# Performance work log

Hardware: AMD Instinct MI355X
Metric: run time of the kernel (lower is better)

## Reference

```python
import jax, jax.numpy as jnp
import numpy as np
import math

D, H, DK, DFF, B, T, K = 512, 8, 64, 2048, 8, 512, 31
P = 2 * T - 1  # rel-pos length


def _ln(x, g, b, eps=1e-5):
    mu = jnp.mean(x, -1, keepdims=True)
    var = jnp.var(x, -1, keepdims=True)
    return (x - mu) * jax.lax.rsqrt(var + eps) * g + b


def _silu(x):
    return x * jax.nn.sigmoid(x)


def _rel_shift(x):
    # x: [B,H,T,P] -> NeMo-style relative shift
    b, h, t, p = x.shape
    x = jnp.pad(x, ((0, 0), (0, 0), (0, 0), (1, 0)))
    x = x.reshape(b, h, p + 1, t)
    return x[:, :, 1:, :].reshape(b, h, t, p)


def _forward(x, pos_emb, ln1_g, ln1_b, ff1_w1, ff1_b1, ff1_w2, ff1_b2,
             lna_g, lna_b, wq, bq, wk, bk, wv, bv, wo, bo, wpos, pbu, pbv,
             lnc_g, lnc_b, pw1_w, pw1_b, dw_w, dw_b, cln_g, cln_b, pw2_w, pw2_b,
             ln2_g, ln2_b, ff2_w1, ff2_b1, ff2_w2, ff2_b2, lno_g, lno_b):
    b, t, d = x.shape
    h, dk = pbu.shape
    # FF1 (half-step residual)
    r = x
    y = _ln(x, ln1_g, ln1_b)
    y = _silu(y @ ff1_w1 + ff1_b1) @ ff1_w2 + ff1_b2
    r = r + 0.5 * y
    # Rel-pos multi-head attention
    y = _ln(r, lna_g, lna_b)
    q = (y @ wq + bq).reshape(b, t, h, dk)
    k = (y @ wk + bk).reshape(b, t, h, dk)
    v = (y @ wv + bv).reshape(b, t, h, dk)
    p = (pos_emb @ wpos).reshape(pos_emb.shape[0], -1, h, dk)[0]  # [P,H,dk]
    ac = jnp.einsum('bthd,bshd->bhts', q + pbu, k)
    bd = jnp.einsum('bthd,phd->bhtp', q + pbv, p)
    bd = _rel_shift(bd)[..., :t]
    attn = jax.nn.softmax((ac + bd) / math.sqrt(dk), axis=-1)
    o = jnp.einsum('bhts,bshd->bthd', attn, v).reshape(b, t, d) @ wo + bo
    r = r + o
    # Conformer convolution module (layer_norm variant)
    y = _ln(r, lnc_g, lnc_b)
    y = y @ pw1_w + pw1_b                       # [B,T,2D] pointwise conv1
    a, g = jnp.split(y, 2, axis=-1)
    y = a * jax.nn.sigmoid(g)                   # GLU over channels
    y = jnp.transpose(y, (0, 2, 1))             # [B,D,T]
    pad = (dw_w.shape[1] - 1) // 2
    y = jax.lax.conv_general_dilated(
        y, dw_w[:, None, :], (1,), [(pad, pad)],
        feature_group_count=d, dimension_numbers=('NCH', 'OIH', 'NCH'))
    y = y + dw_b[None, :, None]
    y = jnp.transpose(y, (0, 2, 1))             # [B,T,D]
    y = _ln(y, cln_g, cln_b)
    y = _silu(y) @ pw2_w + pw2_b                # pointwise conv2
    r = r + y
    # FF2 (half-step residual)
    y = _ln(r, ln2_g, ln2_b)
    y = _silu(y @ ff2_w1 + ff2_b1) @ ff2_w2 + ff2_b2
    r = r + 0.5 * y
    return _ln(r, lno_g, lno_b)


def setup_inputs() -> dict:
    key = jax.random.key(0)
    ks = iter(jax.random.split(key, 64))
    rn = lambda shape, s=0.05: jax.random.normal(next(ks), shape, dtype=jnp.float32) * s
    ones = lambda n: jnp.ones((n,), jnp.float32)
    zeros = lambda n: jnp.zeros((n,), jnp.float32)
    return dict(
        x=jax.random.normal(next(ks), (B, T, D), jnp.float32),
        pos_emb=jax.random.normal(next(ks), (1, P, D), jnp.float32),
        ln1_g=ones(D), ln1_b=zeros(D),
        ff1_w1=rn((D, DFF)), ff1_b1=zeros(DFF), ff1_w2=rn((DFF, D)), ff1_b2=zeros(D),
        lna_g=ones(D), lna_b=zeros(D),
        wq=rn((D, D)), bq=zeros(D), wk=rn((D, D)), bk=zeros(D),
        wv=rn((D, D)), bv=zeros(D), wo=rn((D, D)), bo=zeros(D),
        wpos=rn((D, D)), pbu=rn((H, DK)), pbv=rn((H, DK)),
        lnc_g=ones(D), lnc_b=zeros(D),
        pw1_w=rn((D, 2 * D)), pw1_b=zeros(2 * D),
        dw_w=rn((D, K)), dw_b=zeros(D),
        cln_g=ones(D), cln_b=zeros(D),
        pw2_w=rn((D, D)), pw2_b=zeros(D),
        ln2_g=ones(D), ln2_b=zeros(D),
        ff2_w1=rn((D, DFF)), ff2_b1=zeros(DFF), ff2_w2=rn((DFF, D)), ff2_b2=zeros(D),
        lno_g=ones(D), lno_b=zeros(D))


def reference(x, pos_emb, ln1_g, ln1_b, ff1_w1, ff1_b1, ff1_w2, ff1_b2,
              lna_g, lna_b, wq, bq, wk, bk, wv, bv, wo, bo, wpos, pbu, pbv,
              lnc_g, lnc_b, pw1_w, pw1_b, dw_w, dw_b, cln_g, cln_b, pw2_w, pw2_b,
              ln2_g, ln2_b, ff2_w1, ff2_b1, ff2_w2, ff2_b2, lno_g, lno_b):
    return _forward(x, pos_emb, ln1_g, ln1_b, ff1_w1, ff1_b1, ff1_w2, ff1_b2,
                    lna_g, lna_b, wq, bq, wk, bk, wv, bv, wo, bo, wpos, pbu, pbv,
                    lnc_g, lnc_b, pw1_w, pw1_b, dw_w, dw_b, cln_g, cln_b, pw2_w, pw2_b,
                    ln2_g, ln2_b, ff2_w1, ff2_b1, ff2_w2, ff2_b2, lno_g, lno_b)
```

## Files before the change

### kernel.cpp

```cpp
#include <hip/hip_runtime.h>
#include <hip/hip_bf16.h>

#define Bb 8
#define Tt 512
#define Dd 512
#define Hh 8
#define DKk 64
#define DFFf 2048
#define Pp 1023
#define KCc 31
#define BTt 4096
#define QS 1536

typedef __hip_bfloat16 bf16;
typedef __attribute__((ext_vector_type(8))) short short8;
typedef __attribute__((ext_vector_type(4))) short s4v;
typedef __attribute__((ext_vector_type(4))) float f32x4;

union BFU { __hip_bfloat16 h; short s; };
static __device__ __forceinline__ short bfbits(float f) {
    BFU u; u.h = __float2bfloat16(f); return u.s;
}
static __device__ __forceinline__ float bff(short s) {
    BFU u; u.s = s; return __bfloat162float(u.h);
}
static __device__ __forceinline__ unsigned pk2(float a, float b) {
    return (unsigned)(unsigned short)bfbits(a) | ((unsigned)(unsigned short)bfbits(b) << 16);
}

static __device__ __forceinline__ int dflag(const void* lg) {
    return ((const unsigned*)lg)[0] == 0x3F803F80u;
}

#define GLD16(g, l) __builtin_amdgcn_global_load_lds(                          \
    (const __attribute__((address_space(1))) void*)(g),                        \
    (__attribute__((address_space(3))) void*)(l), 16, 0, 0)

#define XCD_SWZ(bxs, bys)                                                     \
    int nwg_ = gridDim.x * gridDim.y;                                         \
    int w_ = blockIdx.y * gridDim.x + blockIdx.x;                             \
    int sw_ = (w_ & 7) * (nwg_ >> 3) + (w_ >> 3);                             \
    int bxs = sw_ % gridDim.x, bys = sw_ / gridDim.x;

struct CvtDesc { const void* src; unsigned n; unsigned off; unsigned startBlk; };
struct CvtArgs { CvtDesc d[32]; };

__global__ __launch_bounds__(256) void cvt_batch_k(CvtArgs args, int ncv,
                                                   bf16* __restrict__ dst,
                                                   const void* __restrict__ lg) {
    int bid = blockIdx.x;
    int ti = 0;
    while (ti + 1 < ncv && bid >= (int)args.d[ti + 1].startBlk) ti++;
    CvtDesc de = args.d[ti];
    unsigned i = (bid - de.startBlk) * 256u + threadIdx.x;
    if (i >= de.n) return;
    float v;
    if (dflag(lg)) v = __bfloat162float(((const bf16*)de.src)[i]);
    else           v = ((const float*)de.src)[i];
    dst[de.off + i] = __float2bfloat16(v);
}

struct TD { const void* src; unsigned doff, R, C, startBlk; };
struct TArgs { TD d[11]; };

__global__ __launch_bounds__(256) void transpose_batch_k(TArgs ta, bf16* __restrict__ wt,
                                                         const void* __restrict__ lg) {
    int bid = blockIdx.x;
    int ti = 0;
    while (ti + 1 < 11 && bid >= (int)ta.d[ti + 1].startBlk) ti++;
    TD t = ta.d[ti];
    int tile = bid - t.startBlk;
    int ntc = t.C >> 5;
    int tr = tile / ntc, tc = tile % ntc;
    __shared__ short tl[32][33];
    short* out = (short*)wt + t.doff;
    int tx = threadIdx.x & 31, ty = threadIdx.x >> 5;
    int fl = dflag(lg);
#pragma unroll
    for (int i = 0; i < 32; i += 8) {
        size_t idx = (size_t)(tr * 32 + ty + i) * t.C + tc * 32 + tx;
        short v;
        if (fl) v = ((const short*)t.src)[idx];
        else    v = bfbits(((const float*)t.src)[idx]);
        tl[ty + i][tx] = v;
    }
    __syncthreads();
#pragma unroll
    for (int i = 0; i < 32; i += 8)
        out[(size_t)(tc * 32 + ty + i) * t.R + tr * 32 + tx] = tl[tx][ty + i];
}

__global__ __launch_bounds__(256) void prep_misc_k(const void* __restrict__ dww, bf16* __restrict__ dwT,
                                                   const void* __restrict__ bq, const void* __restrict__ bk,
                                                   const void* __restrict__ bv, bf16* __restrict__ bqkv,
                                                   const void* __restrict__ lg) {
    int i = blockIdx.x * 256 + threadIdx.x;
    int fl = dflag(lg);
    if (i < Dd * KCc) {
        int d = i / KCc, j = i % KCc;
        short v = fl ? ((const short*)dww)[i] : bfbits(((const float*)dww)[i]);
        ((short*)dwT)[j * Dd + d] = v;
    } else {
        int j = i - Dd * KCc;
        if (j < QS) {
            const void* s = (j < 512) ? bq : ((j < 1024) ? bk : bv);
            int idx = j & 511;
            short v = fl ? ((const short*)s)[idx] : bfbits(((const float*)s)[idx]);
            ((short*)bqkv)[j] = v;
        }
    }
}

__global__ __launch_bounds__(256) void prep_pf_k(const bf16* __restrict__ pbuf,
                                                 bf16* __restrict__ pF) {
    int h = blockIdx.x >> 6, J = blockIdx.x & 63;
    int idx = threadIdx.x * 4;
    int ksp = idx >> 9;
    int l = (idx >> 3) & 63;
    int e0 = idx & 7;
    int lm = l & 15, qd = l >> 4;
    int prow = J * 16 - 1 + lm;
    s4v v;
    if (prow < 0) {
        v = s4v{0, 0, 0, 0};
    } else {
        v = *(const s4v*)((const short*)pbuf + (size_t)prow * Dd + h * DKk + ksp * 32 + qd * 8 + e0);
    }
    *(s4v*)((short*)pF + ((size_t)h * 64 + J) * 1024 + idx) = v;
}

template <int SILU>
__global__ __launch_bounds__(256) void ln_k(const float* __restrict__ in,
                                            const bf16* __restrict__ g,
                                            const bf16* __restrict__ b,
                                            bf16* __restrict__ out) {
    int row = blockIdx.x;
    int tid = threadIdx.x;
    float2 v = ((const float2*)(in + (size_t)row * Dd))[tid];
    float s = v.x + v.y;
    float ss = v.x * v.x + v.y * v.y;
#pragma unroll
    for (int off = 32; off > 0; off >>= 1) {
        s += __shfl_xor(s, off);
        ss += __shfl_xor(ss, off);
    }
    __shared__ float red[2][4];
    int wid = tid >> 6;
    if ((tid & 63) == 0) { red[0][wid] = s; red[1][wid] = ss; }
    __syncthreads();
    float S = red[0][0] + red[0][1] + red[0][2] + red[0][3];
    float SS = red[1][0] + red[1][1] + red[1][2] + red[1][3];
    float mean = S * (1.0f / Dd);
    float var = SS * (1.0f / Dd) - mean * mean;
    float rstd = rsqrtf(var + 1e-5f);
    unsigned gp = *(const unsigned*)((const short*)g + 2 * tid);
    unsigned bp = *(const unsigned*)((const short*)b + 2 * tid);
    float o0 = (v.x - mean) * rstd * bff((short)(gp & 0xFFFF)) + bff((short)(bp & 0xFFFF));
    float o1 = (v.y - mean) * rstd * bff((short)(gp >> 16)) + bff((short)(bp >> 16));
    if (SILU) {
        o0 = o0 / (1.0f + __expf(-o0));
        o1 = o1 / (1.0f + __expf(-o1));
    }
    *(unsigned*)((short*)out + (size_t)row * Dd + 2 * tid) = pk2(o0, o1);
}

__global__ __launch_bounds__(256) void ln_x_k(const void* __restrict__ x,
                                              const bf16* __restrict__ g,
                                              const bf16* __restrict__ b,
                                              float* __restrict__ r,
                                              bf16* __restrict__ out,
                                              const void* __restrict__ lg) {
    int row = blockIdx.x;
    int tid = threadIdx.x;
    size_t base = (size_t)row * Dd;
    float v0, v1;
    if (dflag(lg)) {
        unsigned xp = *(const unsigned*)((const short*)x + base + 2 * tid);
        v0 = bff((short)(xp & 0xFFFF));
        v1 = bff((short)(xp >> 16));
    } else {
        float2 xv = ((const float2*)((const float*)x + base))[tid];
        v0 = xv.x; v1 = xv.y;
    }
    ((float2*)(r + base))[tid] = make_float2(v0, v1);
    float s = v0 + v1;
    float ss = v0 * v0 + v1 * v1;
#pragma unroll
    for (int off = 32; off > 0; off >>= 1) {
        s += __shfl_xor(s, off);
        ss += __shfl_xor(ss, off);
    }
    __shared__ float red[2][4];
    int wid = tid >> 6;
    if ((tid & 63) == 0) { red[0][wid] = s; red[1][wid] = ss; }
    __syncthreads();
    float S = red[0][0] + red[0][1] + red[0][2] + red[0][3];
    float SS = red[1][0] + red[1][1] + red[1][2] + red[1][3];
    float mean = S * (1.0f / Dd);
    float var = SS * (1.0f / Dd) - mean * mean;
    float rstd = rsqrtf(var + 1e-5f);
    unsigned gp = *(const unsigned*)((const short*)g + 2 * tid);
    unsigned bp = *(const unsigned*)((const short*)b + 2 * tid);
    float o0 = (v0 - mean) * rstd * bff((short)(gp & 0xFFFF)) + bff((short)(bp & 0xFFFF));
    float o1 = (v1 - mean) * rstd * bff((short)(gp >> 16)) + bff((short)(bp >> 16));
    *(unsigned*)((short*)out + base + 2 * tid) = pk2(o0, o1);
}

__global__ __launch_bounds__(256) void ln_out_k(const float* __restrict__ in,
                                                const bf16* __restrict__ g,
                                                const bf16* __restrict__ b,
                                                void* __restrict__ out,
                                                const void* __restrict__ lg) {
    int row = blockIdx.x;
    int tid = threadIdx.x;
    size_t base = (size_t)row * Dd;
    float2 v = ((const float2*)(in + base))[tid];
    float s = v.x + v.y;
    float ss = v.x * v.x + v.y * v.y;
#pragma unroll
    for (int off = 32; off > 0; off >>= 1) {
        s += __shfl_xor(s, off);
        ss += __shfl_xor(ss, off);
    }
    __shared__ float red[2][4];
    int wid = tid >> 6;
    if ((tid & 63) == 0) { red[0][wid] = s; red[1][wid] = ss; }
    __syncthreads();
    float S = red[0][0] + red[0][1] + red[0][2] + red[0][3];
    float SS = red[1][0] + red[1][1] + red[1][2] + red[1][3];
    float mean = S * (1.0f / Dd);
    float var = SS * (1.0f / Dd) - mean * mean;
    float rstd = rsqrtf(var + 1e-5f);
    unsigned gp = *(const unsigned*)((const short*)g + 2 * tid);
    unsigned bp = *(const unsigned*)((const short*)b + 2 * tid);
    float o0 = (v.x - mean) * rstd * bff((short)(gp & 0xFFFF)) + bff((short)(bp & 0xFFFF));
    float o1 = (v.y - mean) * rstd * bff((short)(gp >> 16)) + bff((short)(bp >> 16));
    if (dflag(lg)) {
        *(unsigned*)((short*)out + base + 2 * tid) = pk2(o0, o1);
    } else {
        ((float2*)((float*)out + base))[tid] = make_float2(o0, o1);
    }
}

template <int BM, int BN, int BK, int WM, int WN, typename CT, int ACT, int RES, int VT>
__global__ __launch_bounds__(256) void gemm_mfma_k(const bf16* __restrict__ Abf,
                                                   const bf16* __restrict__ WT,
                                                   const bf16* __restrict__ bias,
                                                   const float* __restrict__ resid,
                                                   CT* __restrict__ C,
                                                   bf16* __restrict__ vt,
                                                   bf16* __restrict__ kf,
                                                   int M, int N, int Kd, float alpha) {
    constexpr int MT = WM / 16, NT = WN / 16;
    constexpr int WX = BN / WN;
    constexpr int CPB = BK / 8;
    constexpr int KS = BK / 32;
    __shared__ __align__(16) short As[BM * BK];
    __shared__ __align__(16) short Bs[BN * BK];
    int tid = threadIdx.x;
    int wid = tid >> 6, lane = tid & 63;
    int lm = lane & 15, quad = lane >> 4;
    int wy = wid / WX, wx = wid % WX;
    XCD_SWZ(bxs, bys);
    int bm = bys * BM, bn = bxs * BN;
    const short* Ag = (const short*)Abf;
    const short* Bg = (const short*)WT;

    f32x4 acc[MT][NT] = {};

    for (int k0 = 0; k0 < Kd; k0 += BK) {
#pragma unroll
        for (int it = 0; it < BM * CPB / 256; it++) {
            int c = it * 256 + tid;
            int row = c / CPB;
            int q = (c % CPB) ^ (row & 7);
            int gr = bm + row;
            if (gr > M - 1) gr = M - 1;
            GLD16(Ag + (size_t)gr * Kd + k0 + q * 8, As + (it * 256 + wid * 64) * 8);
        }
#pragma unroll
        for (int it = 0; it < BN * CPB / 256; it++) {
            int c = it * 256 + tid;
            int row = c / CPB;
            int q = (c % CPB) ^ (row & 7);
            GLD16(Bg + (size_t)(bn + row) * Kd + k0 + q * 8, Bs + (it * 256 + wid * 64) * 8);
        }
        __syncthreads();
        short8 af[MT][KS], bfv[NT][KS];
#pragma unroll
        for (int mt = 0; mt < MT; mt++) {
            int row = wy * WM + mt * 16 + lm;
#pragma unroll
            for (int ks = 0; ks < KS; ks++)
                af[mt][ks] = *(const short8*)&As[row * BK + (((ks * 4 + quad) ^ (row & 7)) * 8)];
        }
#pragma unroll
        for (int nt = 0; nt < NT; nt++) {
            int row = wx * WN + nt * 16 + lm;
#pragma unroll
            for (int ks = 0; ks < KS; ks++)
                bfv[nt][ks] = *(const short8*)&Bs[row * BK + (((ks * 4 + quad) ^ (row & 7)) * 8)];
        }
#pragma unroll
        for (int ks = 0; ks < KS; ks++)
#pragma unroll
            for (int mt = 0; mt < MT; mt++)
#pragma unroll
                for (int nt = 0; nt < NT; nt++)
                    acc[mt][nt] = __builtin_amdgcn_mfma_f32_16x16x32_bf16(af[mt][ks], bfv[nt][ks], acc[mt][nt], 0, 0, 0);
        __syncthreads();
    }

#pragma unroll
    for (int mt = 0; mt < MT; mt++) {
#pragma unroll
        for (int nt = 0; nt < NT; nt++) {
            int gcol = bn + wx * WN + nt * 16 + lm;
            int growb = bm + wy * WM + mt * 16 + quad * 4;
            if (VT && gcol >= 1024) {
                int hd = gcol - 1024;
                int h = hd >> 6, d = hd & 63;
                int b = growb >> 9, tt = growb & 511;
                float bi = bias ? __bfloat162float(bias[gcol]) : 0.f;
                s4v pk;
#pragma unroll
                for (int r = 0; r < 4; r++) pk[r] = bfbits(acc[mt][nt][r] + bi);
                size_t base = (((((size_t)b * 8 + h) * 16 + (tt >> 5)) * 4 + (d >> 4)) * 64 +
                               (((tt >> 3) & 3) * 16 + (d & 15))) * 8 + (tt & 7);
                *(s4v*)((short*)vt + base) = pk;
            } else if (VT && gcol >= 512) {
                int hd = gcol - 512;
                int h = hd >> 6, kk = hd & 63;
                int b = growb >> 9, tt = growb & 511;
                float bi = __bfloat162float(bias[gcol]);
                size_t base2 = ((((size_t)b * 8 + h) * 32 + (tt >> 4)) * 2 + (kk >> 5)) * 512;
                int qd = (kk >> 3) & 3, e = kk & 7;
#pragma unroll
                for (int r = 0; r < 4; r++)
                    ((short*)kf)[base2 + (size_t)(qd * 16 + (tt & 15) + r) * 8 + e] =
                        bfbits(acc[mt][nt][r] + bi);
            } else {
#pragma unroll
                for (int r = 0; r < 4; r++) {
                    int grow = growb + r;
                    if (grow >= M) continue;
                    float v = acc[mt][nt][r];
                    if (bias) v += __bfloat162float(bias[gcol]);
                    if (ACT == 1) v = v / (1.0f + __expf(-v));
                    if (RES == 1) v = resid[(size_t)grow * N + gcol] + alpha * v;
                    C[(size_t)grow * N + gcol] = (CT)v;
                }
            }
        }
    }
}

__global__ __launch_bounds__(256) void gemm_glu_k(const bf16* __restrict__ Abf,
                                                  const bf16* __restrict__ WT,
                                                  const bf16* __restrict__ bias,
                                                  bf16* __restrict__ C) {
    constexpr int BM = 64, BN = 64, BK = 64, WM = 32, WN = 32;
    constexpr int MT = WM / 16, NT = WN / 16, WX = BN / WN, CPB = BK / 8, KS = BK / 32;
    __shared__ __align__(16) short As[BM * BK];
    __shared__ __align__(16) short Bs[2 * BN * BK];
    int tid = threadIdx.x;
    int wid = tid >> 6, lane = tid & 63;
    int lm = lane & 15, quad = lane >> 4;
    int wy = wid / WX, wx = wid % WX;
    XCD_SWZ(bxs, bys);
    int bm = bys * BM, bn = bxs * BN;
    const short* Ag = (const short*)Abf;
    const short* Bg = (const short*)WT;

    f32x4 acc[MT][NT][2] = {};

    for (int k0 = 0; k0 < Dd; k0 += BK) {
#pragma unroll
        for (int it = 0; it < BM * CPB / 256; it++) {
            int c = it * 256 + tid;
            int row = c / CPB;
            int q = (c % CPB) ^ (row & 7);
            GLD16(Ag + (size_t)(bm + row) * Dd + k0 + q * 8, As + (it * 256 + wid * 64) * 8);
        }
#pragma unroll
        for (int it = 0; it < 2 * BN * CPB / 256; it++) {
            int c = it * 256 + tid;
            int row = c / CPB;
            int q = (c % CPB) ^ (row & 7);
            int wrow = (row < BN) ? (bn + row) : (512 + bn + row - BN);
            GLD16(Bg + (size_t)wrow * Dd + k0 + q * 8, Bs + (it * 256 + wid * 64) * 8);
        }
        __syncthreads();
        short8 af[MT][KS], bfv[NT][2][KS];
#pragma unroll
        for (int mt = 0; mt < MT; mt++) {
            int row = wy * WM + mt * 16 + lm;
#pragma unroll
            for (int ks = 0; ks < KS; ks++)
                af[mt][ks] = *(const short8*)&As[row * BK + (((ks * 4 + quad) ^ (row & 7)) * 8)];
        }
#pragma unroll
        for (int nt = 0; nt < NT; nt++) {
#pragma unroll
            for (int hf = 0; hf < 2; hf++) {
                int row = hf * BN + wx * WN + nt * 16 + lm;
#pragma unroll
                for (int ks = 0; ks < KS; ks++)
                    bfv[nt][hf][ks] = *(const short8*)&Bs[row * BK + (((ks * 4 + quad) ^ (row & 7)) * 8)];
            }
        }
#pragma unroll
        for (int ks = 0; ks < KS; ks++)
#pragma unroll
            for (int mt = 0; mt < MT; mt++)
#pragma unroll
                for (int nt = 0; nt < NT; nt++) {
                    acc[mt][nt][0] = __builtin_amdgcn_mfma_f32_16x16x32_bf16(af[mt][ks], bfv[nt][0][ks], acc[mt][nt][0], 0, 0, 0);
                    acc[mt][nt][1] = __builtin_amdgcn_mfma_f32_16x16x32_bf16(af[mt][ks], bfv[nt][1][ks], acc[mt][nt][1], 0, 0, 0);
                }
        __syncthreads();
    }

#pragma unroll
    for (int mt = 0; mt < MT; mt++) {
#pragma unroll
        for (int nt = 0; nt < NT; nt++) {
#pragma unroll
            for (int r = 0; r < 4; r++) {
                int grow = bm + wy * WM + mt * 16 + quad * 4 + r;
                int gcol = bn + wx * WN + nt * 16 + lm;
                float va = acc[mt][nt][0][r] + __bfloat162float(bias[gcol]);
                float vg = acc[mt][nt][1][r] + __bfloat162float(bias[512 + gcol]);
                float v = va / (1.0f + __expf(-vg));
                C[(size_t)grow * Dd + gcol] = __float2bfloat16(v);
            }
        }
    }
}

#define PST 520

__global__ __launch_bounds__(256, 4) void attn_mfma_k(const bf16* __restrict__ qkv,
                                                      const bf16* __restrict__ kF,
                                                      const bf16* __restrict__ pF,
                                                      const bf16* __restrict__ vF,
                                                      const bf16* __restrict__ pbu,
                                                      const bf16* __restrict__ pbv,
                                                      bf16* __restrict__ out) {
    __shared__ __align__(16) short Pl[16 * PST];
    __shared__ __align__(16) float redm[16][4];
    __shared__ __align__(16) float reds[16][4];
    int tid = threadIdx.x;
    int wid = tid >> 6;
    int lane = tid & 63;
    int lm = lane & 15;
    int quad = lane >> 4;
    int bidx = (blockIdx.x & 7) * 256 + (blockIdx.x >> 3);
    int b = bidx >> 8;
    int h = (bidx >> 5) & 7;
    int t0 = (bidx & 31) * 16;

    const short* qkvs = (const short*)qkv;

    short8 qu[2], qv[2];
    {
        size_t rowbase = ((size_t)(b * Tt + t0 + lm) * QS) + h * DKk;
        const short* pbus = (const short*)pbu + h * DKk + quad * 8;
        const short* pbvs = (const short*)pbv + h * DKk + quad * 8;
#pragma unroll
        for (int ksp = 0; ksp < 2; ksp++) {
            short8 raw = *(const short8*)(qkvs + rowbase + ksp * 32 + quad * 8);
            short8 bu = *(const short8*)(pbus + ksp * 32);
            short8 bv = *(const short8*)(pbvs + ksp * 32);
#pragma unroll
            for (int j = 0; j < 8; j++) {
                float qf = bff(raw[j]);
                qu[ksp][j] = bfbits(qf + bff(bu[j]));
                qv[ksp][j] = bfbits(qf + bff(bv[j]));
            }
        }
    }

    const float scale = 0.125f;
    const short* kFs = (const short*)kF + ((size_t)(b * 8 + h) * 32) * 1024;
    const short* pFs = (const short*)pF + ((size_t)h * 64) * 1024;
    int Jbase = 32 - (t0 >> 4) + wid * 8;

    f32x4 dprev = {0.f, 0.f, 0.f, 0.f};
    {
        const short* pa = pFs + (size_t)(Jbase - 1) * 1024 + lane * 8;
        dprev = __builtin_amdgcn_mfma_f32_16x16x32_bf16(qv[0], *(const short8*)pa, dprev, 0, 0, 0);
        dprev = __builtin_amdgcn_mfma_f32_16x16x32_bf16(qv[1], *(const short8*)(pa + 512), dprev, 0, 0, 0);
    }

    f32x4 sreg[8];
#pragma unroll
    for (int i = 0; i < 8; i++) {
        int st = wid * 8 + i;
        f32x4 ac = {0.f, 0.f, 0.f, 0.f};
        f32x4 dcur = {0.f, 0.f, 0.f, 0.f};
        const short* ka = kFs + (size_t)st * 1024 + lane * 8;
        const short* pa = pFs + (size_t)(Jbase + i) * 1024 + lane * 8;
        ac = __builtin_amdgcn_mfma_f32_16x16x32_bf16(qu[0], *(const short8*)ka, ac, 0, 0, 0);
        ac = __builtin_amdgcn_mfma_f32_16x16x32_bf16(qu[1], *(const short8*)(ka + 512), ac, 0, 0, 0);
        dcur = __builtin_amdgcn_mfma_f32_16x16x32_bf16(qv[0], *(const short8*)pa, dcur, 0, 0, 0);
        dcur = __builtin_amdgcn_mfma_f32_16x16x32_bf16(qv[1], *(const short8*)(pa + 512), dcur, 0, 0, 0);
#pragma unroll
        for (int r = 0; r < 4; r++) {
            int m = quad * 4 + r;
            int j = (lm - m) & 15;
            int srcl = quad * 16 + j;
            float b2 = __shfl(dcur[r], srcl, 64);
            float b1 = __shfl(dprev[r], srcl, 64);
            float bd = (lm >= m) ? b2 : b1;
            sreg[i][r] = scale * (ac[r] + bd);
        }
        dprev = dcur;
    }

    float mrow[4];
#pragma unroll
    for (int r = 0; r < 4; r++) {
        float m = sreg[0][r];
#pragma unroll
        for (int i = 1; i < 8; i++) m = fmaxf(m, sreg[i][r]);
#pragma unroll
        for (int off = 1; off < 16; off <<= 1) m = fmaxf(m, __shfl_xor(m, off));
        mrow[r] = m;
    }
    if (lm < 4) {
        float v = (lm == 0) ? mrow[0] : (lm == 1) ? mrow[1] : (lm == 2) ? mrow[2] : mrow[3];
        redm[quad * 4 + lm][wid] = v;
    }
    __syncthreads();

    float gm[4], srow[4];
#pragma unroll
    for (int r = 0; r < 4; r++) {
        float4 mv = *(const float4*)&redm[quad * 4 + r][0];
        gm[r] = fmaxf(fmaxf(mv.x, mv.y), fmaxf(mv.z, mv.w));
        srow[r] = 0.f;
    }
#pragma unroll
    for (int i = 0; i < 8; i++) {
        int col = (wid * 8 + i) * 16 + lm;
#pragma unroll
        for (int r = 0; r < 4; r++) {
            float e = __expf(sreg[i][r] - gm[r]);
            srow[r] += e;
            Pl[(quad * 4 + r) * PST + col] = bfbits(e);
        }
    }
#pragma unroll
    for (int r = 0; r < 4; r++) {
#pragma unroll
        for (int off = 1; off < 16; off <<= 1) srow[r] += __shfl_xor(srow[r], off);
    }
    if (lm < 4) {
        float v = (lm == 0) ? srow[0] : (lm == 1) ? srow[1] : (lm == 2) ? srow[2] : srow[3];
        reds[quad * 4 + lm][wid] = v;
    }
    __syncthreads();

    float lsum[4];
#pragma unroll
    for (int r = 0; r < 4; r++) {
        float4 sv = *(const float4*)&reds[quad * 4 + r][0];
        lsum[r] = (sv.x + sv.y) + (sv.z + sv.w);
    }

    int d0 = wid * 16;
    const short* va = (const short*)vF + (size_t)(b * 8 + h) * 32768 + wid * 512 + lane * 8;
    const short* parow = Pl + (size_t)lm * PST;
    f32x4 o0 = {0.f, 0.f, 0.f, 0.f};
    f32x4 o1 = {0.f, 0.f, 0.f, 0.f};
#pragma unroll
    for (int ksp = 0; ksp < 16; ksp += 2) {
        short8 a0 = *(const short8*)(parow + ksp * 32 + quad * 8);
        short8 v0 = *(const short8*)(va + (size_t)ksp * 2048);
        short8 a1 = *(const short8*)(parow + (ksp + 1) * 32 + quad * 8);
        short8 v1 = *(const short8*)(va + (size_t)(ksp + 1) * 2048);
        o0 = __builtin_amdgcn_mfma_f32_16x16x32_bf16(a0, v0, o0, 0, 0, 0);
        o1 = __builtin_amdgcn_mfma_f32_16x16x32_bf16(a1, v1, o1, 0, 0, 0);
    }
    f32x4 o = o0 + o1;
    short* os = (short*)out;
#pragma unroll
    for (int r = 0; r < 4; r++) {
        int m = quad * 4 + r;
        os[((size_t)(b * Tt + t0 + m) * Dd) + h * DKk + d0 + lm] = bfbits(o[r] / lsum[r]);
    }
}

__global__ __launch_bounds__(256) void dwconv_ln_k(const bf16* __restrict__ in,
                                                   const bf16* __restrict__ wT,
                                                   const bf16* __restrict__ bdw,
                                                   const bf16* __restrict__ g,
                                                   const bf16* __restrict__ bb,
                                                   bf16* __restrict__ out) {
    int row = blockIdx.x * 4 + (threadIdx.x >> 6);
    int lane = threadIdx.x & 63;
    int d0 = lane * 8;
    int t = row & 511, b = row >> 9;
    const short* ins = (const short*)in + (size_t)b * Tt * Dd;
    const short* wts = (const short*)wT;
    float acc[8];
    short8 bv = *(const short8*)((const short*)bdw + d0);
#pragma unroll
    for (int e = 0; e < 8; e++) acc[e] = bff(bv[e]);
#pragma unroll
    for (int j = 0; j < KCc; j++) {
        int tt = t + j - 15;
        if (tt < 0 || tt >= Tt) continue;
        short8 iv = *(const short8*)(ins + (size_t)tt * Dd + d0);
        short8 wv = *(const short8*)(wts + j * Dd + d0);
#pragma unroll
        for (int e = 0; e < 8; e++) acc[e] += bff(iv[e]) * bff(wv[e]);
    }
    float s = 0.f, ss = 0.f;
#pragma unroll
    for (int e = 0; e < 8; e++) { s += acc[e]; ss += acc[e] * acc[e]; }
#pragma unroll
    for (int off = 32; off > 0; off >>= 1) {
        s += __shfl_xor(s, off);
        ss += __shfl_xor(ss, off);
    }
    float mean = s * (1.0f / Dd);
    float var = ss * (1.0f / Dd) - mean * mean;
    float rstd = rsqrtf(var + 1e-5f);
    short8 gv = *(const short8*)((const short*)g + d0);
    short8 bbv = *(const short8*)((const short*)bb + d0);
    short8 ov;
#pragma unroll
    for (int e = 0; e < 8; e++) {
        float o = (acc[e] - mean) * rstd * bff(gv[e]) + bff(bbv[e]);
        o = o / (1.0f + __expf(-o));
        ov[e] = bfbits(o);
    }
    *(short8*)((short*)out + (size_t)row * Dd + d0) = ov;
}

extern "C" void kernel_launch(void* const* d_in, const int* in_sizes, int n_in,
                              void* d_out, int out_size, void* d_ws, size_t ws_size,
                              hipStream_t stream) {
    char* base = (char*)d_ws;
    bf16* wb = (bf16*)(base + 256);

    size_t woff[39];
    size_t acc = 0;
    for (int i = 1; i < 39; i++) { woff[i] = acc; acc += (size_t)in_sizes[i]; }
    size_t wbytes = (2 * acc + 255) & ~(size_t)255;

    const size_t NBT = (size_t)BTt * Dd;
    float* r   = (float*)((char*)wb + wbytes);
    bf16* a    = (bf16*)((char*)r + NBT * 4);
    bf16* big  = a + NBT;
    bf16* pbuf = big + (size_t)BTt * DFFf;
    bf16* wt   = pbuf + (size_t)Pp * Dd;

    const void* lg = d_in[2];

    bf16* c_pos   = wb + woff[1];
    bf16* c_ln1g  = wb + woff[2],  *c_ln1b = wb + woff[3];
    bf16* c_f1b1  = wb + woff[5];
    bf16* c_f1b2  = wb + woff[7];
    bf16* c_lnag  = wb + woff[8],  *c_lnab = wb + woff[9];
    bf16* c_bo    = wb + woff[17];
    bf16* c_pbu   = wb + woff[19], *c_pbv  = wb + woff[20];
    bf16* c_lncg  = wb + woff[21], *c_lncb = wb + woff[22];
    bf16* c_p1b   = wb + woff[24];
    bf16* c_dwb   = wb + woff[26];
    bf16* c_clng  = wb + woff[27], *c_clnb = wb + woff[28];
    bf16* c_p2b   = wb + woff[30];
    bf16* c_ln2g  = wb + woff[31], *c_ln2b = wb + woff[32];
    bf16* c_f2b1  = wb + woff[34];
    bf16* c_f2b2  = wb + woff[36];
    bf16* c_lnog  = wb + woff[37], *c_lnob = wb + woff[38];

    const int tin[11]  = {4, 6, 10, 12, 14, 16, 18, 23, 29, 33, 35};
    const unsigned tR[11] = {512, 2048, 512, 512, 512, 512, 512, 512, 512, 512, 2048};
    const unsigned tC[11] = {2048, 512, 512, 512, 512, 512, 512, 1024, 512, 2048, 512};
    size_t toff[11]; size_t tacc = 0;
    for (int i = 0; i < 11; i++) { toff[i] = tacc; tacc += (size_t)tR[i] * tC[i]; }
    bf16* t_f1w1 = wt + toff[0];
    bf16* t_f1w2 = wt + toff[1];
    bf16* t_wqkv = wt + toff[2];
    bf16* t_wo   = wt + toff[5];
    bf16* t_wpos = wt + toff[6];
    bf16* t_p1w  = wt + toff[7];
    bf16* t_p2w  = wt + toff[8];
    bf16* t_f2w1 = wt + toff[9];
    bf16* t_f2w2 = wt + toff[10];
    bf16* bias_qkv = wt + tacc;
    bf16* dwT      = bias_qkv + QS;
    bf16* vTb      = dwT + KCc * Dd;
    bf16* kFb      = vTb + (size_t)2097152;
    bf16* pFb      = kFb + (size_t)2097152;

    dim3 blk(256);

    bool skip[39] = {};
    for (int i = 0; i < 11; i++) skip[tin[i]] = true;
    skip[11] = skip[13] = skip[15] = skip[25] = true;
    CvtArgs ca;
    int ncv = 0;
    unsigned blkacc = 0;
    for (int i = 1; i < 39; i++) {
        if (skip[i]) continue;
        ca.d[ncv].src = d_in[i];
        ca.d[ncv].n = (unsigned)in_sizes[i];
        ca.d[ncv].off = (unsigned)woff[i];
        ca.d[ncv].startBlk = blkacc;
        blkacc += (unsigned)((in_sizes[i] + 255) / 256);
        ncv++;
    }
    cvt_batch_k<<<blkacc, blk, 0, stream>>>(ca, ncv, wb, lg);

    TArgs ta;
    unsigned tblk = 0;
    for (int i = 0; i < 11; i++) {
        ta.d[i].src = d_in[tin[i]];
        ta.d[i].doff = (unsigned)toff[i];
        ta.d[i].R = tR[i];
        ta.d[i].C = tC[i];
        ta.d[i].startBlk = tblk;
        tblk += (tR[i] >> 5) * (tC[i] >> 5);
    }
    transpose_batch_k<<<tblk, blk, 0, stream>>>(ta, wt, lg);
    prep_misc_k<<<(Dd * KCc + QS + 255) / 256, blk, 0, stream>>>(
        d_in[25], dwT, d_in[11], d_in[13], d_in[15], bias_qkv, lg);

    auto g128 = [](int M, int N) { return dim3(N / 128, M / 128); };
    auto g64  = [](int M, int N) { return dim3(N / 64, (M + 63) / 64); };

    ln_x_k<<<BTt, blk, 0, stream>>>(d_in[0], c_ln1g, c_ln1b, r, a, lg);
    gemm_mfma_k<128, 128, 64, 64, 64, bf16, 1, 0, 0><<<g128(BTt, DFFf), blk, 0, stream>>>(
        a, t_f1w1, c_f1b1, nullptr, big, nullptr, nullptr, BTt, DFFf, Dd, 0.f);
    gemm_mfma_k<64, 64, 128, 32, 32, float, 0, 1, 0><<<g64(BTt, Dd), blk, 0, stream>>>(
        big, t_f1w2, c_f1b2, r, r, nullptr, nullptr, BTt, Dd, DFFf, 0.5f);

    bf16* qkvb = big;
    bf16* cb   = big + 3 * NBT;
    ln_k<0><<<BTt, blk, 0, stream>>>(r, c_lnag, c_lnab, a);
    gemm_mfma_k<128, 64, 64, 64, 32, bf16, 0, 0, 1><<<dim3(QS / 64, BTt / 128), blk, 0, stream>>>(
        a, t_wqkv, bias_qkv, nullptr, qkvb, vTb, kFb, BTt, QS, Dd, 0.f);
    gemm_mfma_k<64, 64, 64, 32, 32, bf16, 0, 0, 0><<<g64(Pp, Dd), blk, 0, stream>>>(
        c_pos, t_wpos, nullptr, nullptr, pbuf, nullptr, nullptr, Pp, Dd, Dd, 0.f);
    prep_pf_k<<<8 * 64, blk, 0, stream>>>(pbuf, pFb);
    attn_mfma_k<<<Bb * Hh * (Tt / 16), blk, 0, stream>>>(qkvb, kFb, pFb, vTb, c_pbu, c_pbv, cb);
    gemm_mfma_k<64, 64, 64, 32, 32, float, 0, 1, 0><<<g64(BTt, Dd), blk, 0, stream>>>(
        cb, t_wo, c_bo, r, r, nullptr, nullptr, BTt, Dd, Dd, 1.0f);

    bf16* gluo = big + 2 * NBT;
    ln_k<0><<<BTt, blk, 0, stream>>>(r, c_lncg, c_lncb, a);
    gemm_glu_k<<<dim3(Dd / 64, BTt / 64), blk, 0, stream>>>(a, t_p1w, c_p1b, gluo);
    dwconv_ln_k<<<BTt / 4, blk, 0, stream>>>(gluo, dwT, c_dwb, c_clng, c_clnb, a);
    gemm_mfma_k<64, 64, 64, 32, 32, float, 0, 1, 0><<<g64(BTt, Dd), blk, 0, stream>>>(
        a, t_p2w, c_p2b, r, r, nullptr, nullptr, BTt, Dd, Dd, 1.0f);

    ln_k<0><<<BTt, blk, 0, stream>>>(r, c_ln2g, c_ln2b, a);
    gemm_mfma_k<128, 128, 64, 64, 64, bf16, 1, 0, 0><<<g128(BTt, DFFf), blk, 0, stream>>>(
        a, t_f2w1, c_f2b1, nullptr, big, nullptr, nullptr, BTt, DFFf, Dd, 0.f);
    gemm_mfma_k<64, 64, 128, 32, 32, float, 0, 1, 0><<<g64(BTt, Dd), blk, 0, stream>>>(
        big, t_f2w2, c_f2b2, r, r, nullptr, nullptr, BTt, Dd, DFFf, 0.5f);

    ln_out_k<<<BTt, blk, 0, stream>>>(r, c_lnog, c_lnob, d_out, lg);
}
```

Before: 399.0 us.

## Write Q and pos projections directly in MFMA fragment layouts; stage attention output

The QKV GEMM epilogue now writes Q in the same fragment-tiled layout as K, so attention loads Q fragments contiguously. The positional projection GEMM writes straight into the shifted pF layout, with the zero row filled in prep_misc_k, which removes the separate prep_pf kernel and its intermediate buffer. The attention output is staged through shared memory so global writes are coalesced vector stores. The FF1/FF2 up-projection GEMMs also use BK=128. Risks are more scattered epilogue stores, an extra buffer, and larger shared-memory use in the FF GEMMs.

```diff
diff --git a/kernel.cpp b/kernel.cpp
--- a/kernel.cpp
+++ b/kernel.cpp
@@ -93,6 +93,7 @@
 __global__ __launch_bounds__(256) void prep_misc_k(const void* __restrict__ dww, bf16* __restrict__ dwT,
                                                    const void* __restrict__ bq, const void* __restrict__ bk,
                                                    const void* __restrict__ bv, bf16* __restrict__ bqkv,
+                                                   bf16* __restrict__ pF,
                                                    const void* __restrict__ lg) {
     int i = blockIdx.x * 256 + threadIdx.x;
     int fl = dflag(lg);
@@ -100,33 +101,19 @@
         int d = i / KCc, j = i % KCc;
         short v = fl ? ((const short*)dww)[i] : bfbits(((const float*)dww)[i]);
         ((short*)dwT)[j * Dd + d] = v;
+    } else if (i < Dd * KCc + QS) {
+        int j = i - Dd * KCc;
+        const void* s = (j < 512) ? bq : ((j < 1024) ? bk : bv);
+        int idx = j & 511;
+        short v = fl ? ((const short*)s)[idx] : bfbits(((const float*)s)[idx]);
+        ((short*)bqkv)[j] = v;
     } else {
-        int j = i - Dd * KCc;
-        if (j < QS) {
-            const void* s = (j < 512) ? bq : ((j < 1024) ? bk : bv);
-            int idx = j & 511;
-            short v = fl ? ((const short*)s)[idx] : bfbits(((const float*)s)[idx]);
-            ((short*)bqkv)[j] = v;
-        }
-    }
-}
-
-__global__ __launch_bounds__(256) void prep_pf_k(const bf16* __restrict__ pbuf,
-                                                 bf16* __restrict__ pF) {
-    int h = blockIdx.x >> 6, J = blockIdx.x & 63;
-    int idx = threadIdx.x * 4;
-    int ksp = idx >> 9;
-    int l = (idx >> 3) & 63;
-    int e0 = idx & 7;
-    int lm = l & 15, qd = l >> 4;
-    int prow = J * 16 - 1 + lm;
-    s4v v;
-    if (prow < 0) {
-        v = s4v{0, 0, 0, 0};
-    } else {
-        v = *(const s4v*)((const short*)pbuf + (size_t)prow * Dd + h * DKk + ksp * 32 + qd * 8 + e0);
-    }
-    *(s4v*)((short*)pF + ((size_t)h * 64 + J) * 1024 + idx) = v;
+        int j2 = i - Dd * KCc - QS;
+        if (j2 < 512) {
+            int h = j2 >> 6, ksp = (j2 >> 5) & 1, qd = (j2 >> 3) & 3, e = j2 & 7;
+            ((short*)pF)[(size_t)h * 65536 + ksp * 512 + qd * 128 + e] = 0;
+        }
+    }
 }
 
 template <int SILU>
@@ -250,6 +237,7 @@
                                                    CT* __restrict__ C,
                                                    bf16* __restrict__ vt,
                                                    bf16* __restrict__ kf,
+                                                   bf16* __restrict__ qf,
                                                    int M, int N, int Kd, float alpha) {
     constexpr int MT = WM / 16, NT = WN / 16;
     constexpr int WX = BN / WN;
@@ -317,18 +305,18 @@
         for (int nt = 0; nt < NT; nt++) {
             int gcol = bn + wx * WN + nt * 16 + lm;
             int growb = bm + wy * WM + mt * 16 + quad * 4;
-            if (VT && gcol >= 1024) {
+            if (VT == 1 && gcol >= 1024) {
                 int hd = gcol - 1024;
                 int h = hd >> 6, d = hd & 63;
                 int b = growb >> 9, tt = growb & 511;
-                float bi = bias ? __bfloat162float(bias[gcol]) : 0.f;
+                float bi = __bfloat162float(bias[gcol]);
                 s4v pk;
 #pragma unroll
                 for (int r = 0; r < 4; r++) pk[r] = bfbits(acc[mt][nt][r] + bi);
                 size_t base = (((((size_t)b * 8 + h) * 16 + (tt >> 5)) * 4 + (d >> 4)) * 64 +
                                (((tt >> 3) & 3) * 16 + (d & 15))) * 8 + (tt & 7);
                 *(s4v*)((short*)vt + base) = pk;
-            } else if (VT && gcol >= 512) {
+            } else if (VT == 1 && gcol >= 512) {
                 int hd = gcol - 512;
                 int h = hd >> 6, kk = hd & 63;
                 int b = growb >> 9, tt = growb & 511;
@@ -339,6 +327,28 @@
                 for (int r = 0; r < 4; r++)
                     ((short*)kf)[base2 + (size_t)(qd * 16 + (tt & 15) + r) * 8 + e] =
                         bfbits(acc[mt][nt][r] + bi);
+            } else if (VT == 1) {
+                int h = gcol >> 6, kk = gcol & 63;
+                int b = growb >> 9, tt = growb & 511;
+                float bi = __bfloat162float(bias[gcol]);
+                size_t base2 = ((((size_t)b * 8 + h) * 32 + (tt >> 4)) * 2 + (kk >> 5)) * 512;
+                int qd = (kk >> 3) & 3, e = kk & 7;
+#pragma unroll
+                for (int r = 0; r < 4; r++)
+                    ((short*)qf)[base2 + (size_t)(qd * 16 + (tt & 15) + r) * 8 + e] =
+                        bfbits(acc[mt][nt][r] + bi);
+            } else if (VT == 2) {
+                int h = gcol >> 6, kk = gcol & 63;
+                int ksp = kk >> 5, qd = (kk >> 3) & 3, e = kk & 7;
+#pragma unroll
+                for (int r = 0; r < 4; r++) {
+                    int grow = growb + r;
+                    if (grow >= M) continue;
+                    int p1 = grow + 1;
+                    int J = p1 >> 4, lmz = p1 & 15;
+                    ((short*)vt)[(size_t)(h * 64 + J) * 1024 + ksp * 512 + (qd * 16 + lmz) * 8 + e] =
+                        bfbits(acc[mt][nt][r]);
+                }
             } else {
 #pragma unroll
                 for (int r = 0; r < 4; r++) {
@@ -439,8 +449,9 @@
 }
 
 #define PST 520
-
-__global__ __launch_bounds__(256, 4) void attn_mfma_k(const bf16* __restrict__ qkv,
+#define OST 72
+
+__global__ __launch_bounds__(256, 4) void attn_mfma_k(const bf16* __restrict__ qF,
                                                       const bf16* __restrict__ kF,
                                                       const bf16* __restrict__ pF,
                                                       const bf16* __restrict__ vF,
@@ -460,23 +471,22 @@
     int h = (bidx >> 5) & 7;
     int t0 = (bidx & 31) * 16;
 
-    const short* qkvs = (const short*)qkv;
-
     short8 qu[2], qv[2];
     {
-        size_t rowbase = ((size_t)(b * Tt + t0 + lm) * QS) + h * DKk;
+        const short* qa = (const short*)qF +
+            ((size_t)((b * 8 + h) * 32 + (t0 >> 4)) * 2) * 512 + lane * 8;
         const short* pbus = (const short*)pbu + h * DKk + quad * 8;
         const short* pbvs = (const short*)pbv + h * DKk + quad * 8;
 #pragma unroll
         for (int ksp = 0; ksp < 2; ksp++) {
-            short8 raw = *(const short8*)(qkvs + rowbase + ksp * 32 + quad * 8);
+            short8 raw = *(const short8*)(qa + ksp * 512);
             short8 bu = *(const short8*)(pbus + ksp * 32);
             short8 bv = *(const short8*)(pbvs + ksp * 32);
 #pragma unroll
             for (int j = 0; j < 8; j++) {
-                float qf = bff(raw[j]);
-                qu[ksp][j] = bfbits(qf + bff(bu[j]));
-                qv[ksp][j] = bfbits(qf + bff(bv[j]));
+                float qf2 = bff(raw[j]);
+                qu[ksp][j] = bfbits(qf2 + bff(bu[j]));
+                qv[ksp][j] = bfbits(qf2 + bff(bv[j]));
             }
         }
     }
@@ -584,11 +594,16 @@
         o1 = __builtin_amdgcn_mfma_f32_16x16x32_bf16(a1, v1, o1, 0, 0, 0);
     }
     f32x4 o = o0 + o1;
-    short* os = (short*)out;
-#pragma unroll
-    for (int r = 0; r < 4; r++) {
-        int m = quad * 4 + r;
-        os[((size_t)(b * Tt + t0 + m) * Dd) + h * DKk + d0 + lm] = bfbits(o[r] / lsum[r]);
+
+    __syncthreads();
+#pragma unroll
+    for (int r = 0; r < 4; r++)
+        Pl[(quad * 4 + r) * OST + d0 + lm] = bfbits(o[r] / lsum[r]);
+    __syncthreads();
+    {
+        int row = tid >> 4, c4 = (tid & 15) * 4;
+        s4v ov = *(const s4v*)&Pl[row * OST + c4];
+        *(s4v*)((short*)out + (size_t)(b * Tt + t0 + row) * Dd + h * DKk + c4) = ov;
     }
 }
 
@@ -696,6 +711,7 @@
     bf16* vTb      = dwT + KCc * Dd;
     bf16* kFb      = vTb + (size_t)2097152;
     bf16* pFb      = kFb + (size_t)2097152;
+    bf16* qFb      = pFb + (size_t)524288;
 
     dim3 blk(256);
 
@@ -727,42 +743,40 @@
         tblk += (tR[i] >> 5) * (tC[i] >> 5);
     }
     transpose_batch_k<<<tblk, blk, 0, stream>>>(ta, wt, lg);
-    prep_misc_k<<<(Dd * KCc + QS + 255) / 256, blk, 0, stream>>>(
-        d_in[25], dwT, d_in[11], d_in[13], d_in[15], bias_qkv, lg);
+    prep_misc_k<<<(Dd * KCc + QS + 512 + 255) / 256, blk, 0, stream>>>(
+        d_in[25], dwT, d_in[11], d_in[13], d_in[15], bias_qkv, pFb, lg);
 
     auto g128 = [](int M, int N) { return dim3(N / 128, M / 128); };
     auto g64  = [](int M, int N) { return dim3(N / 64, (M + 63) / 64); };
 
     ln_x_k<<<BTt, blk, 0, stream>>>(d_in[0], c_ln1g, c_ln1b, r, a, lg);
-    gemm_mfma_k<128, 128, 64, 64, 64, bf16, 1, 0, 0><<<g128(BTt, DFFf), blk, 0, stream>>>(
-        a, t_f1w1, c_f1b1, nullptr, big, nullptr, nullptr, BTt, DFFf, Dd, 0.f);
+    gemm_mfma_k<128, 128, 128, 64, 64, bf16, 1, 0, 0><<<g128(BTt, DFFf), blk, 0, stream>>>(
+        a, t_f1w1, c_f1b1, nullptr, big, nullptr, nullptr, nullptr, BTt, DFFf, Dd, 0.f);
     gemm_mfma_k<64, 64, 128, 32, 32, float, 0, 1, 0><<<g64(BTt, Dd), blk, 0, stream>>>(
-        big, t_f1w2, c_f1b2, r, r, nullptr, nullptr, BTt, Dd, DFFf, 0.5f);
-
-    bf16* qkvb = big;
-    bf16* cb   = big + 3 * NBT;
+        big, t_f1w2, c_f1b2, r, r, nullptr, nullptr, nullptr, BTt, Dd, DFFf, 0.5f);
+
+    bf16* cb = big + 3 * NBT;
     ln_k<0><<<BTt, blk, 0, stream>>>(r, c_lnag, c_lnab, a);
     gemm_mfma_k<128, 64, 64, 64, 32, bf16, 0, 0, 1><<<dim3(QS / 64, BTt / 128), blk, 0, stream>>>(
-        a, t_wqkv, bias_qkv, nullptr, qkvb, vTb, kFb, BTt, QS, Dd, 0.f);
-    gemm_mfma_k<64, 64, 64, 32, 32, bf16, 0, 0, 0><<<g64(Pp, Dd), blk, 0, stream>>>(
-        c_pos, t_wpos, nullptr, nullptr, pbuf, nullptr, nullptr, Pp, Dd, Dd, 0.f);
-    prep_pf_k<<<8 * 64, blk, 0, stream>>>(pbuf, pFb);
-    attn_mfma_k<<<Bb * Hh * (Tt / 16), blk, 0, stream>>>(qkvb, kFb, pFb, vTb, c_pbu, c_pbv, cb);
+        a, t_wqkv, bias_qkv, nullptr, (bf16*)nullptr, vTb, kFb, qFb, BTt, QS, Dd, 0.f);
+    gemm_mfma_k<64, 64, 64, 32, 32, bf16, 0, 0, 2><<<g64(Pp, Dd), blk, 0, stream>>>(
+        c_pos, t_wpos, nullptr, nullptr, (bf16*)nullptr, pFb, nullptr, nullptr, Pp, Dd, Dd, 0.f);
+    attn_mfma_k<<<Bb * Hh * (Tt / 16), blk, 0, stream>>>(qFb, kFb, pFb, vTb, c_pbu, c_pbv, cb);
     gemm_mfma_k<64, 64, 64, 32, 32, float, 0, 1, 0><<<g64(BTt, Dd), blk, 0, stream>>>(
-        cb, t_wo, c_bo, r, r, nullptr, nullptr, BTt, Dd, Dd, 1.0f);
+        cb, t_wo, c_bo, r, r, nullptr, nullptr, nullptr, BTt, Dd, Dd, 1.0f);
 
     bf16* gluo = big + 2 * NBT;
     ln_k<0><<<BTt, blk, 0, stream>>>(r, c_lncg, c_lncb, a);
     gemm_glu_k<<<dim3(Dd / 64, BTt / 64), blk, 0, stream>>>(a, t_p1w, c_p1b, gluo);
     dwconv_ln_k<<<BTt / 4, blk, 0, stream>>>(gluo, dwT, c_dwb, c_clng, c_clnb, a);
     gemm_mfma_k<64, 64, 64, 32, 32, float, 0, 1, 0><<<g64(BTt, Dd), blk, 0, stream>>>(
-        a, t_p2w, c_p2b, r, r, nullptr, nullptr, BTt, Dd, Dd, 1.0f);
+        a, t_p2w, c_p2b, r, r, nullptr, nullptr, nullptr, BTt, Dd, Dd, 1.0f);
 
     ln_k<0><<<BTt, blk, 0, stream>>>(r, c_ln2g, c_ln2b, a);
-    gemm_mfma_k<128, 128, 64, 64, 64, bf16, 1, 0, 0><<<g128(BTt, DFFf), blk, 0, stream>>>(
-        a, t_f2w1, c_f2b1, nullptr, big, nullptr, nullptr, BTt, DFFf, Dd, 0.f);
+    gemm_mfma_k<128, 128, 128, 64, 64, bf16, 1, 0, 0><<<g128(BTt, DFFf), blk, 0, stream>>>(
+        a, t_f2w1, c_f2b1, nullptr, big, nullptr, nullptr, nullptr, BTt, DFFf, Dd, 0.f);
     gemm_mfma_k<64, 64, 128, 32, 32, float, 0, 1, 0><<<g64(BTt, Dd), blk, 0, stream>>>(
-        big, t_f2w2, c_f2b2, r, r, nullptr, nullptr, BTt, Dd, DFFf, 0.5f);
+        big, t_f2w2, c_f2b2, r, r, nullptr, nullptr, nullptr, BTt, Dd, DFFf, 0.5f);
 
     ln_out_k<<<BTt, blk, 0, stream>>>(r, c_lnog, c_lnob, d_out, lg);
 }
```

After: 390.6 us. -2.1%, faster.
